# Performance work log

Measured on AMD Instinct MI355X. Metric: run time of the kernel, lower is better.

The kernel has to match this reference:

```python
import jax, jax.numpy as jnp
import numpy as np

B, S, D, H = 4, 2048, 1024, 16
HD = D // H  # head_dim = 64


def setup_inputs() -> dict:
    key = jax.random.key(0)
    ks = jax.random.split(key, 11)
    s = 1.0 / np.sqrt(D)
    return {
        "Q": jax.random.normal(ks[0], (B, S, D), dtype=jnp.float32),
        "K": jax.random.normal(ks[1], (B, S, D), dtype=jnp.float32),
        "V": jax.random.normal(ks[2], (B, S, D), dtype=jnp.float32),
        "Wq": jax.random.normal(ks[3], (D, D), dtype=jnp.float32) * s,
        "bq": jnp.zeros((D,), dtype=jnp.float32),
        "Wk": jax.random.normal(ks[4], (D, D), dtype=jnp.float32) * s,
        "bk": jnp.zeros((D,), dtype=jnp.float32),
        "Wv": jax.random.normal(ks[5], (D, D), dtype=jnp.float32) * s,
        "bv": jnp.zeros((D,), dtype=jnp.float32),
        "Wo": jax.random.normal(ks[6], (D, D), dtype=jnp.float32) * s,
        "bo": jnp.zeros((D,), dtype=jnp.float32),
    }


def _split_heads(x):
    # [B, S, D] -> [B, H, S, HD]
    b, s, _ = x.shape
    return x.reshape(b, s, H, HD).transpose(0, 2, 1, 3)


def reference(Q, K, V, Wq, bq, Wk, bk, Wv, bv, Wo, bo):
    q = _split_heads(Q @ Wq + bq)  # [B,H,S,HD]
    k = _split_heads(K @ Wk + bk)
    v = _split_heads(V @ Wv + bv)
    scale = 1.0 / jnp.sqrt(jnp.float32(HD))
    scores = jnp.einsum('bhqd,bhkd->bhqk', q, k) * scale  # [B,H,S,S]
    attn = jax.nn.softmax(scores, axis=-1)
    out = jnp.einsum('bhqk,bhkd->bhqd', attn, v)  # [B,H,S,HD]
    out = out.transpose(0, 2, 1, 3).reshape(Q.shape[0], -1, D)  # [B,S,D]
    return out @ Wo + bo
```

## Files before the change

kernel.cpp:

```cpp
#include <hip/hip_runtime.h>
#include <hip/hip_bf16.h>

typedef unsigned short u16;
typedef unsigned int u32;
typedef u16 u16x4 __attribute__((ext_vector_type(4)));
typedef u16 u16x8 __attribute__((ext_vector_type(8)));
typedef u32 u32x4 __attribute__((ext_vector_type(4)));
typedef float f32x4 __attribute__((ext_vector_type(4)));
typedef float f32x16 __attribute__((ext_vector_type(16)));
typedef __bf16 bf16x8 __attribute__((ext_vector_type(8)));

#define MFMA16(A, B, C) __builtin_amdgcn_mfma_f32_16x16x32_bf16( \
    __builtin_bit_cast(bf16x8, (A)), __builtin_bit_cast(bf16x8, (B)), (C), 0, 0, 0)
#define MFMA32(A, B, C) __builtin_amdgcn_mfma_f32_32x32x16_bf16( \
    __builtin_bit_cast(bf16x8, (A)), __builtin_bit_cast(bf16x8, (B)), (C), 0, 0, 0)

__device__ __forceinline__ u16 f2bf(float f) {
    u32 u = __float_as_uint(f);
    u += 0x7fffu + ((u >> 16) & 1u);
    return (u16)(u >> 16);
}

__device__ __forceinline__ u32 cvtpk(float lo, float hi) {
    u32 d;
    asm("v_cvt_pk_bf16_f32 %0, %1, %2" : "=v"(d) : "v"(lo), "v"(hi));
    return d;
}

__device__ __forceinline__ void gll16(const void* g, void* l) {
    __builtin_amdgcn_global_load_lds(
        (const __attribute__((address_space(1))) void*)g,
        (__attribute__((address_space(3))) void*)l, 16, 0, 0);
}

__global__ void f2bf3(const float* __restrict__ a0, const float* __restrict__ a1,
                      const float* __restrict__ a2, u16* __restrict__ o0,
                      u16* __restrict__ o1, u16* __restrict__ o2, int n4) {
    const float* in = (blockIdx.y == 0) ? a0 : (blockIdx.y == 1) ? a1 : a2;
    u16* out = (blockIdx.y == 0) ? o0 : (blockIdx.y == 1) ? o1 : o2;
    int i = blockIdx.x * blockDim.x + threadIdx.x;
    int stride = gridDim.x * blockDim.x;
    for (; i < n4; i += stride) {
        float4 v = ((const float4*)in)[i];
        u16x4 o;
        o[0] = f2bf(v.x); o[1] = f2bf(v.y); o[2] = f2bf(v.z); o[3] = f2bf(v.w);
        ((u16x4*)out)[i] = o;
    }
}

__global__ void cvt_wt(const float* __restrict__ W0, const float* __restrict__ W1,
                       const float* __restrict__ W2, const float* __restrict__ W3,
                       u16* __restrict__ T0, u16* __restrict__ T1,
                       u16* __restrict__ T2, u16* __restrict__ T3) {
    const int z = blockIdx.z;
    const float* W = (z == 0) ? W0 : (z == 1) ? W1 : (z == 2) ? W2 : W3;
    u16* T = (z == 0) ? T0 : (z == 1) ? T1 : (z == 2) ? T2 : T3;
    __shared__ float tile[64][65];
    const int n0 = blockIdx.x * 64, k0 = blockIdx.y * 64;
    const int tx = threadIdx.x & 63, ty = threadIdx.x >> 6;
#pragma unroll
    for (int i = 0; i < 16; ++i) {
        int r = i * 4 + ty;
        tile[r][tx] = W[(size_t)(k0 + r) * 1024 + n0 + tx];
    }
    __syncthreads();
#pragma unroll
    for (int i = 0; i < 16; ++i) {
        int r = i * 4 + ty;
        T[(size_t)(n0 + r) * 1024 + k0 + tx] = f2bf(tile[tx][r]);
    }
}

__device__ __forceinline__ void gemm_core(
    const u16* __restrict__ A, const u16* __restrict__ Bt,
    const float* __restrict__ bias, void* __restrict__ out,
    int mode, float scale, int bm, int bn, u16* lAs, u16* lBs) {
    const int tid = threadIdx.x, lane = tid & 63, wid = tid >> 6;
    const int wr = wid >> 1, wc = wid & 1;
    const int l15 = lane & 15, l16 = lane >> 4;

    f32x4 acc[4][4];
#pragma unroll
    for (int i = 0; i < 4; ++i)
#pragma unroll
        for (int j = 0; j < 4; ++j) acc[i][j] = f32x4{0.f, 0.f, 0.f, 0.f};

    const char* Ab = (const char*)A;
    const char* Bb = (const char*)Bt;
    char* ldsA = (char*)lAs;
    char* ldsB = (char*)lBs;
    const int rA0 = (wid * 4) * 8 + (lane >> 3);
    const int ci = ((lane & 7) ^ (lane >> 3)) * 16;

    for (int k0 = 0; k0 < 1024; k0 += 64) {
        __syncthreads();
#pragma unroll
        for (int c = 0; c < 4; ++c) {
            int row = rA0 + c * 8;
            gll16(Ab + ((size_t)(bm + row) * 1024 + k0) * 2 + ci, ldsA + (wid * 4 + c) * 1024);
            gll16(Bb + ((size_t)(bn + row) * 1024 + k0) * 2 + ci, ldsB + (wid * 4 + c) * 1024);
        }
        asm volatile("s_waitcnt vmcnt(0)" ::: "memory");
        __syncthreads();

#pragma unroll
        for (int kk = 0; kk < 2; ++kk) {
            u16x8 af[4], bf[4];
#pragma unroll
            for (int mi = 0; mi < 4; ++mi) {
                int row = wr * 64 + mi * 16 + l15;
                int cg = kk * 4 + l16;
                af[mi] = *(const u16x8*)(ldsA + row * 128 + ((cg ^ (row & 7)) * 16));
            }
#pragma unroll
            for (int ni = 0; ni < 4; ++ni) {
                int row = wc * 64 + ni * 16 + l15;
                int cg = kk * 4 + l16;
                bf[ni] = *(const u16x8*)(ldsB + row * 128 + ((cg ^ (row & 7)) * 16));
            }
#pragma unroll
            for (int mi = 0; mi < 4; ++mi)
#pragma unroll
                for (int ni = 0; ni < 4; ++ni)
                    acc[mi][ni] = MFMA16(af[mi], bf[ni], acc[mi][ni]);
        }
    }

    const int row0 = bm + wr * 64, col0 = bn + wc * 64;
#pragma unroll
    for (int ni = 0; ni < 4; ++ni) {
        int col = col0 + ni * 16 + l15;
        float bv = bias[col];
#pragma unroll
        for (int mi = 0; mi < 4; ++mi) {
#pragma unroll
            for (int r = 0; r < 4; ++r) {
                int row = row0 + mi * 16 + l16 * 4 + r;
                float v = (acc[mi][ni][r] + bv) * scale;
                if (mode == 2) {
                    ((float*)out)[(size_t)row * 1024 + col] = v;
                } else if (mode == 0) {
                    int b = row >> 11, s = row & 2047, h = col >> 6, d = col & 63;
                    ((u16*)out)[(((size_t)(b * 16 + h)) * 2048 + s) * 64 + d] = f2bf(v);
                } else {
                    int b = row >> 11, s = row & 2047, h = col >> 6, d = col & 63;
                    ((u16*)out)[(((size_t)(b * 16 + h)) * 64 + d) * 2048 + s] = f2bf(v);
                }
            }
        }
    }
}

__device__ __forceinline__ void xcd_decode(int wg, int& bm, int& bn) {
    int xcd = wg & 7, pos = wg >> 3;
    bm = (xcd * 8 + (pos >> 3)) * 128;
    bn = (pos & 7) * 128;
}

__global__ __launch_bounds__(256, 3) void gemm_qkv(
    const u16* __restrict__ XQ, const u16* __restrict__ XK, const u16* __restrict__ XV,
    const u16* __restrict__ WQ, const u16* __restrict__ WK, const u16* __restrict__ WV,
    const float* __restrict__ bq, const float* __restrict__ bk, const float* __restrict__ bv,
    u16* __restrict__ qo, u16* __restrict__ ko, u16* __restrict__ vo, float qscale) {
    __shared__ u16 lAs[128 * 64];
    __shared__ u16 lBs[128 * 64];
    const int z = blockIdx.z;
    const u16* A = (z == 0) ? XQ : (z == 1) ? XK : XV;
    const u16* Bt = (z == 0) ? WQ : (z == 1) ? WK : WV;
    const float* bias = (z == 0) ? bq : (z == 1) ? bk : bv;
    u16* out = (z == 0) ? qo : (z == 1) ? ko : vo;
    const int mode = (z == 2) ? 1 : 0;
    const float scale = (z == 0) ? qscale : 1.0f;
    int bm, bn;
    xcd_decode(blockIdx.y * 8 + blockIdx.x, bm, bn);
    gemm_core(A, Bt, bias, out, mode, scale, bm, bn, lAs, lBs);
}

__global__ __launch_bounds__(256, 3) void gemm_out(
    const u16* __restrict__ A, const u16* __restrict__ Bt,
    const float* __restrict__ bias, float* __restrict__ out) {
    __shared__ u16 lAs[128 * 64];
    __shared__ u16 lBs[128 * 64];
    int bm, bn;
    xcd_decode(blockIdx.y * 8 + blockIdx.x, bm, bn);
    gemm_core(A, Bt, bias, out, 2, 1.0f, bm, bn, lAs, lBs);
}

__global__ __launch_bounds__(256, 4) void attn_fwd(
    const u16* __restrict__ qh, const u16* __restrict__ kh,
    const u16* __restrict__ vth, u16* __restrict__ ao) {
    __shared__ u16 lK[2][64 * 64];
    __shared__ u16 lV[2][64 * 64];
    const int tid = threadIdx.x, lane = tid & 63, wid = tid >> 6;
    const int l31 = lane & 31, l32 = lane >> 5;
    const int wg = blockIdx.x;
    const int xcd = wg & 7, pos = wg >> 3;
    const int bh = xcd * 8 + (pos >> 4);
    const int xblk = pos & 15;
    const int q0 = xblk * 128 + wid * 32;
    const char* kb = (const char*)(kh + (size_t)bh * 2048 * 64);
    const char* vb = (const char*)(vth + (size_t)bh * 64 * 2048);
    const u16* qb = qh + (size_t)bh * 2048 * 64;

    u16x8 qf[4];
#pragma unroll
    for (int kc = 0; kc < 4; ++kc)
        qf[kc] = *(const u16x8*)(qb + (size_t)(q0 + l31) * 64 + kc * 16 + l32 * 8);

    float m_run = 0.f, l_run = 0.f;
    f32x16 oacc[2] = {};

    char* ldsK = (char*)lK;
    char* ldsV = (char*)lV;
    const int srow = wid * 16 + (lane >> 3);
    const int sci = ((lane & 7) ^ (lane >> 3)) * 16;

#define STAGE(kv0, bo) do { \
    _Pragma("unroll") \
    for (int c = 0; c < 2; ++c) { \
        int row = srow + c * 8; \
        gll16(kb + (size_t)((kv0) + row) * 128 + sci, ldsK + (bo) + (wid * 2 + c) * 1024); \
        gll16(vb + (size_t)row * 4096 + (size_t)(kv0) * 2 + sci, ldsV + (bo) + (wid * 2 + c) * 1024); \
    } } while (0)

    STAGE(0, 0);
    int cur = 0;

    for (int it = 0; it < 32; ++it) {
        if (it < 31) {
            STAGE((it + 1) * 64, (cur ^ 1) * 8192);
            asm volatile("s_waitcnt vmcnt(4)" ::: "memory");
        } else {
            asm volatile("s_waitcnt vmcnt(0)" ::: "memory");
        }
        __syncthreads();
        const char* K_ = ldsK + cur * 8192;
        const char* V_ = ldsV + cur * 8192;

        f32x16 s[2] = {};
        __builtin_amdgcn_s_setprio(1);
#pragma unroll
        for (int kc = 0; kc < 4; ++kc) {
#pragma unroll
            for (int sub = 0; sub < 2; ++sub) {
                int row = sub * 32 + l31;
                int cg = kc * 2 + l32;
                u16x8 kf = *(const u16x8*)(K_ + row * 128 + ((cg ^ (row & 7)) * 16));
                s[sub] = MFMA32(kf, qf[kc], s[sub]);
            }
        }
        __builtin_amdgcn_s_setprio(0);

        float p0[16], p1[16];
#pragma unroll
        for (int r = 0; r < 16; ++r) p0[r] = __builtin_amdgcn_exp2f(s[0][r] - m_run);
#pragma unroll
        for (int r = 0; r < 16; ++r) p1[r] = __builtin_amdgcn_exp2f(s[1][r] - m_run);

        float t8[8];
#pragma unroll
        for (int i = 0; i < 8; ++i)
            t8[i] = fmaxf(fmaxf(s[0][i], s[0][i + 8]), fmaxf(s[1][i], s[1][i + 8]));
        float pm = fmaxf(fmaxf(fmaxf(t8[0], t8[4]), fmaxf(t8[1], t8[5])),
                         fmaxf(fmaxf(t8[2], t8[6]), fmaxf(t8[3], t8[7])));
        pm = fmaxf(pm, __shfl_xor(pm, 32));

        if (!__all(pm <= m_run + 8.f)) {
            float mnew = fmaxf(m_run, pm);
            float f = __builtin_amdgcn_exp2f(m_run - mnew);
            m_run = mnew;
            l_run *= f;
#pragma unroll
            for (int r = 0; r < 16; ++r) p0[r] = __builtin_amdgcn_exp2f(s[0][r] - mnew);
#pragma unroll
            for (int r = 0; r < 16; ++r) p1[r] = __builtin_amdgcn_exp2f(s[1][r] - mnew);
#pragma unroll
            for (int r = 0; r < 16; ++r) {
                int rq = ((r & 3) + 8 * (r >> 2)) + 4 * l32;
                float fr = __shfl(f, rq);
                oacc[0][r] *= fr;
                oacc[1][r] *= fr;
            }
        }

        u16x8 pa[2][2];
#pragma unroll
        for (int c2 = 0; c2 < 2; ++c2) {
            u32 x0 = cvtpk(p0[c2 * 8 + 0], p0[c2 * 8 + 1]);
            u32 x1 = cvtpk(p0[c2 * 8 + 2], p0[c2 * 8 + 3]);
            u32 y0 = cvtpk(p0[c2 * 8 + 4], p0[c2 * 8 + 5]);
            u32 y1 = cvtpk(p0[c2 * 8 + 6], p0[c2 * 8 + 7]);
            asm("v_permlane32_swap_b32 %0, %1" : "+v"(x0), "+v"(y0));
            asm("v_permlane32_swap_b32 %0, %1" : "+v"(x1), "+v"(y1));
            u32x4 wa = {x0, x1, y0, y1};
            pa[0][c2] = __builtin_bit_cast(u16x8, wa);
            u32 z0 = cvtpk(p1[c2 * 8 + 0], p1[c2 * 8 + 1]);
            u32 z1 = cvtpk(p1[c2 * 8 + 2], p1[c2 * 8 + 3]);
            u32 v0 = cvtpk(p1[c2 * 8 + 4], p1[c2 * 8 + 5]);
            u32 v1 = cvtpk(p1[c2 * 8 + 6], p1[c2 * 8 + 7]);
            asm("v_permlane32_swap_b32 %0, %1" : "+v"(z0), "+v"(v0));
            asm("v_permlane32_swap_b32 %0, %1" : "+v"(z1), "+v"(v1));
            u32x4 wb = {z0, z1, v0, v1};
            pa[1][c2] = __builtin_bit_cast(u16x8, wb);
        }

        float a8[8];
#pragma unroll
        for (int i = 0; i < 8; ++i)
            a8[i] = (p0[i] + p0[i + 8]) + (p1[i] + p1[i + 8]);
        float ls = ((a8[0] + a8[4]) + (a8[1] + a8[5])) +
                   ((a8[2] + a8[6]) + (a8[3] + a8[7]));
        ls += __shfl_xor(ls, 32);
        l_run += ls;

        __builtin_amdgcn_s_setprio(1);
#pragma unroll
        for (int dsub = 0; dsub < 2; ++dsub) {
#pragma unroll
            for (int sub = 0; sub < 2; ++sub) {
#pragma unroll
                for (int c2 = 0; c2 < 2; ++c2) {
                    int row = dsub * 32 + l31;
                    int cg = sub * 4 + c2 * 2 + l32;
                    u16x8 vf = *(const u16x8*)(V_ + row * 128 + ((cg ^ (row & 7)) * 16));
                    oacc[dsub] = MFMA32(pa[sub][c2], vf, oacc[dsub]);
                }
            }
        }
        __builtin_amdgcn_s_setprio(0);
        __syncthreads();
        cur ^= 1;
    }
#undef STAGE

    const int b = bh >> 4, h = bh & 15;
    float inv = 1.f / l_run;
#pragma unroll
    for (int r = 0; r < 16; ++r) {
        int rq = ((r & 3) + 8 * (r >> 2)) + 4 * l32;
        float fr = __shfl(inv, rq);
        int sq = q0 + rq;
#pragma unroll
        for (int dsub = 0; dsub < 2; ++dsub) {
            int d = dsub * 32 + l31;
            ao[((size_t)(b * 2048 + sq)) * 1024 + h * 64 + d] = f2bf(oacc[dsub][r] * fr);
        }
    }
}

extern "C" void kernel_launch(void* const* d_in, const int* in_sizes, int n_in,
                              void* d_out, int out_size, void* d_ws, size_t ws_size,
                              hipStream_t stream) {
    const float* Q  = (const float*)d_in[0];
    const float* K  = (const float*)d_in[1];
    const float* V  = (const float*)d_in[2];
    const float* Wq = (const float*)d_in[3];
    const float* bq = (const float*)d_in[4];
    const float* Wk = (const float*)d_in[5];
    const float* bk = (const float*)d_in[6];
    const float* Wv = (const float*)d_in[7];
    const float* bv = (const float*)d_in[8];
    const float* Wo = (const float*)d_in[9];
    const float* bo = (const float*)d_in[10];

    char* ws = (char*)d_ws;
    const size_t MB = 1024u * 1024u;
    u16* XQ  = (u16*)(ws);
    u16* XK  = (u16*)(ws + 16 * MB);
    u16* XV  = (u16*)(ws + 32 * MB);
    u16* WTQ = (u16*)(ws + 48 * MB);
    u16* WTK = (u16*)(ws + 50 * MB);
    u16* WTV = (u16*)(ws + 52 * MB);
    u16* WTO = (u16*)(ws + 54 * MB);
    u16* qhp = (u16*)(ws + 56 * MB);
    u16* khp = (u16*)(ws + 72 * MB);
    u16* vtp = (u16*)(ws + 88 * MB);
    u16* aop = XQ;

    const float qscale = 0.125f * 1.44269504088896f;

    f2bf3<<<dim3(2048, 3), 256, 0, stream>>>(Q, K, V, XQ, XK, XV, 2097152);
    cvt_wt<<<dim3(16, 16, 4), 256, 0, stream>>>(Wq, Wk, Wv, Wo, WTQ, WTK, WTV, WTO);

    gemm_qkv<<<dim3(8, 64, 3), 256, 0, stream>>>(XQ, XK, XV, WTQ, WTK, WTV,
                                                 bq, bk, bv, qhp, khp, vtp, qscale);

    attn_fwd<<<1024, 256, 0, stream>>>(qhp, khp, vtp, aop);

    gemm_out<<<dim3(8, 64), 256, 0, stream>>>(aop, WTO, bo, (float*)d_out);
}
```

Measured before the change: 213.2 us.

## Rewrite projection GEMMs as 8-wave 256x128 tiles with double-buffered LDS pipeline

The QKV and output projection GEMMs move from 4-wave 128x128 blocks with a single-buffered load/sync loop to 8-wave 256x128 blocks. Global-to-LDS loads for the next K tile are double-buffered and interleaved with MFMA phases using barriers and s_setprio. The goal is to hide global load latency behind matrix math and to reuse each B tile across more rows. In exchange it uses 96KB of LDS per block, allows one block per CU, and relies on a fixed barrier schedule that leaves less occupancy to hide stalls.

```diff
diff --git a/kernel.cpp b/kernel.cpp
--- a/kernel.cpp
+++ b/kernel.cpp
@@ -71,60 +71,87 @@
     }
 }
 
-__device__ __forceinline__ void gemm_core(
+__device__ __forceinline__ void gemm8_core(
     const u16* __restrict__ A, const u16* __restrict__ Bt,
     const float* __restrict__ bias, void* __restrict__ out,
-    int mode, float scale, int bm, int bn, u16* lAs, u16* lBs) {
+    int mode, float scale, int bm, int bn, char* ldsA, char* ldsB) {
     const int tid = threadIdx.x, lane = tid & 63, wid = tid >> 6;
     const int wr = wid >> 1, wc = wid & 1;
     const int l15 = lane & 15, l16 = lane >> 4;
-
-    f32x4 acc[4][4];
-#pragma unroll
-    for (int i = 0; i < 4; ++i)
-#pragma unroll
-        for (int j = 0; j < 4; ++j) acc[i][j] = f32x4{0.f, 0.f, 0.f, 0.f};
-
     const char* Ab = (const char*)A;
     const char* Bb = (const char*)Bt;
-    char* ldsA = (char*)lAs;
-    char* ldsB = (char*)lBs;
-    const int rA0 = (wid * 4) * 8 + (lane >> 3);
-    const int ci = ((lane & 7) ^ (lane >> 3)) * 16;
-
-    for (int k0 = 0; k0 < 1024; k0 += 64) {
-        __syncthreads();
-#pragma unroll
-        for (int c = 0; c < 4; ++c) {
-            int row = rA0 + c * 8;
-            gll16(Ab + ((size_t)(bm + row) * 1024 + k0) * 2 + ci, ldsA + (wid * 4 + c) * 1024);
-            gll16(Bb + ((size_t)(bn + row) * 1024 + k0) * 2 + ci, ldsB + (wid * 4 + c) * 1024);
-        }
-        asm volatile("s_waitcnt vmcnt(0)" ::: "memory");
-        __syncthreads();
-
-#pragma unroll
-        for (int kk = 0; kk < 2; ++kk) {
-            u16x8 af[4], bf[4];
-#pragma unroll
-            for (int mi = 0; mi < 4; ++mi) {
-                int row = wr * 64 + mi * 16 + l15;
-                int cg = kk * 4 + l16;
-                af[mi] = *(const u16x8*)(ldsA + row * 128 + ((cg ^ (row & 7)) * 16));
-            }
-#pragma unroll
-            for (int ni = 0; ni < 4; ++ni) {
-                int row = wc * 64 + ni * 16 + l15;
-                int cg = kk * 4 + l16;
-                bf[ni] = *(const u16x8*)(ldsB + row * 128 + ((cg ^ (row & 7)) * 16));
-            }
-#pragma unroll
-            for (int mi = 0; mi < 4; ++mi)
-#pragma unroll
-                for (int ni = 0; ni < 4; ++ni)
-                    acc[mi][ni] = MFMA16(af[mi], bf[ni], acc[mi][ni]);
-        }
-    }
+    const int srow8 = wid * 8 + (lane >> 3);
+    const int sc = ((lane & 7) ^ (lane >> 3)) * 16;
+
+    f32x4 acc[4][4];
+#pragma unroll
+    for (int i = 0; i < 4; ++i)
+#pragma unroll
+        for (int j = 0; j < 4; ++j) acc[i][j] = f32x4{0.f, 0.f, 0.f, 0.f};
+
+#define SA_(t, d, c) gll16(Ab + ((size_t)(bm + (c) * 64 + srow8) * 1024 + (t) * 64) * 2 + sc, \
+                           ldsA + (d) * 32768 + (c) * 8192 + wid * 1024)
+#define SB_(t, d, c) gll16(Bb + ((size_t)(bn + (c) * 64 + srow8) * 1024 + (t) * 64) * 2 + sc, \
+                           ldsB + (d) * 16384 + (c) * 8192 + wid * 1024)
+#define LDA_(d, kk, dst) _Pragma("unroll") \
+    for (int mi = 0; mi < 4; ++mi) { \
+        int row = wr * 64 + mi * 16 + l15; \
+        int cg = (kk) * 4 + l16; \
+        dst[mi] = *(const u16x8*)(ldsA + (d) * 32768 + row * 128 + ((cg ^ (row & 7)) * 16)); }
+#define LDB_(d, kk, dst) _Pragma("unroll") \
+    for (int ni = 0; ni < 4; ++ni) { \
+        int row = wc * 64 + ni * 16 + l15; \
+        int cg = (kk) * 4 + l16; \
+        dst[ni] = *(const u16x8*)(ldsB + (d) * 16384 + row * 128 + ((cg ^ (row & 7)) * 16)); }
+#define MM_(af, bf, nh) _Pragma("unroll") \
+    for (int mi = 0; mi < 4; ++mi) \
+        _Pragma("unroll") for (int nj = 0; nj < 2; ++nj) \
+            acc[mi][(nh) * 2 + nj] = MFMA16(af[mi], bf[(nh) * 2 + nj], acc[mi][(nh) * 2 + nj]);
+
+#define HALF_(d, tp) do { \
+    asm volatile("s_waitcnt vmcnt(0)" ::: "memory"); \
+    __builtin_amdgcn_s_barrier(); \
+    __builtin_amdgcn_sched_barrier(0); \
+    u16x8 a0[4], b0[4], a1[4], b1[4]; \
+    LDA_(d, 0, a0); LDB_(d, 0, b0); \
+    if ((tp) < 16) { SA_(tp, (d) ^ 1, 0); SA_(tp, (d) ^ 1, 1); } \
+    __builtin_amdgcn_s_barrier(); \
+    __builtin_amdgcn_s_setprio(1); \
+    MM_(a0, b0, 0); \
+    __builtin_amdgcn_s_setprio(0); \
+    __builtin_amdgcn_s_barrier(); \
+    LDA_(d, 1, a1); LDB_(d, 1, b1); \
+    if ((tp) < 16) { SA_(tp, (d) ^ 1, 2); SA_(tp, (d) ^ 1, 3); } \
+    __builtin_amdgcn_s_barrier(); \
+    __builtin_amdgcn_s_setprio(1); \
+    MM_(a0, b0, 1); \
+    __builtin_amdgcn_s_setprio(0); \
+    __builtin_amdgcn_s_barrier(); \
+    if ((tp) < 16) { SB_(tp, (d) ^ 1, 0); SB_(tp, (d) ^ 1, 1); } \
+    __builtin_amdgcn_s_barrier(); \
+    __builtin_amdgcn_s_setprio(1); \
+    MM_(a1, b1, 0); \
+    __builtin_amdgcn_s_setprio(0); \
+    __builtin_amdgcn_s_barrier(); \
+    __builtin_amdgcn_s_setprio(1); \
+    MM_(a1, b1, 1); \
+    __builtin_amdgcn_s_setprio(0); \
+    __builtin_amdgcn_s_barrier(); \
+} while (0)
+
+    SA_(0, 0, 0); SA_(0, 0, 1); SA_(0, 0, 2); SA_(0, 0, 3);
+    SB_(0, 0, 0); SB_(0, 0, 1);
+
+    for (int i = 0; i < 8; ++i) {
+        HALF_(0, 2 * i + 1);
+        HALF_(1, 2 * i + 2);
+    }
+#undef HALF_
+#undef MM_
+#undef LDB_
+#undef LDA_
+#undef SB_
+#undef SA_
 
     const int row0 = bm + wr * 64, col0 = bn + wc * 64;
 #pragma unroll
@@ -151,20 +178,20 @@
     }
 }
 
-__device__ __forceinline__ void xcd_decode(int wg, int& bm, int& bn) {
+__device__ __forceinline__ void xcd_decode256(int wg, int& bm, int& bn) {
     int xcd = wg & 7, pos = wg >> 3;
-    bm = (xcd * 8 + (pos >> 3)) * 128;
+    bm = (xcd * 4 + (pos >> 3)) * 256;
     bn = (pos & 7) * 128;
 }
 
-__global__ __launch_bounds__(256, 3) void gemm_qkv(
+__global__ __launch_bounds__(512, 1) void gemm_qkv(
     const u16* __restrict__ XQ, const u16* __restrict__ XK, const u16* __restrict__ XV,
     const u16* __restrict__ WQ, const u16* __restrict__ WK, const u16* __restrict__ WV,
     const float* __restrict__ bq, const float* __restrict__ bk, const float* __restrict__ bv,
     u16* __restrict__ qo, u16* __restrict__ ko, u16* __restrict__ vo, float qscale) {
-    __shared__ u16 lAs[128 * 64];
-    __shared__ u16 lBs[128 * 64];
-    const int z = blockIdx.z;
+    __shared__ char ldsA[65536];
+    __shared__ char ldsB[32768];
+    const int z = blockIdx.y;
     const u16* A = (z == 0) ? XQ : (z == 1) ? XK : XV;
     const u16* Bt = (z == 0) ? WQ : (z == 1) ? WK : WV;
     const float* bias = (z == 0) ? bq : (z == 1) ? bk : bv;
@@ -172,18 +199,18 @@
     const int mode = (z == 2) ? 1 : 0;
     const float scale = (z == 0) ? qscale : 1.0f;
     int bm, bn;
-    xcd_decode(blockIdx.y * 8 + blockIdx.x, bm, bn);
-    gemm_core(A, Bt, bias, out, mode, scale, bm, bn, lAs, lBs);
-}
-
-__global__ __launch_bounds__(256, 3) void gemm_out(
+    xcd_decode256(blockIdx.x, bm, bn);
+    gemm8_core(A, Bt, bias, out, mode, scale, bm, bn, ldsA, ldsB);
+}
+
+__global__ __launch_bounds__(512, 1) void gemm_out(
     const u16* __restrict__ A, const u16* __restrict__ Bt,
     const float* __restrict__ bias, float* __restrict__ out) {
-    __shared__ u16 lAs[128 * 64];
-    __shared__ u16 lBs[128 * 64];
+    __shared__ char ldsA[65536];
+    __shared__ char ldsB[32768];
     int bm, bn;
-    xcd_decode(blockIdx.y * 8 + blockIdx.x, bm, bn);
-    gemm_core(A, Bt, bias, out, 2, 1.0f, bm, bn, lAs, lBs);
+    xcd_decode256(blockIdx.x, bm, bn);
+    gemm8_core(A, Bt, bias, out, 2, 1.0f, bm, bn, ldsA, ldsB);
 }
 
 __global__ __launch_bounds__(256, 4) void attn_fwd(
@@ -382,10 +409,10 @@
     f2bf3<<<dim3(2048, 3), 256, 0, stream>>>(Q, K, V, XQ, XK, XV, 2097152);
     cvt_wt<<<dim3(16, 16, 4), 256, 0, stream>>>(Wq, Wk, Wv, Wo, WTQ, WTK, WTV, WTO);
 
-    gemm_qkv<<<dim3(8, 64, 3), 256, 0, stream>>>(XQ, XK, XV, WTQ, WTK, WTV,
-                                                 bq, bk, bv, qhp, khp, vtp, qscale);
+    gemm_qkv<<<dim3(256, 3), 512, 0, stream>>>(XQ, XK, XV, WTQ, WTK, WTV,
+                                               bq, bk, bv, qhp, khp, vtp, qscale);
 
     attn_fwd<<<1024, 256, 0, stream>>>(qhp, khp, vtp, aop);
 
-    gemm_out<<<dim3(8, 64), 256, 0, stream>>>(aop, WTO, bo, (float*)d_out);
-}
+    gemm_out<<<256, 512, 0, stream>>>(aop, WTO, bo, (float*)d_out);
+}
```

Result: slower. 224.3 us (+5.2%).

## Fuse fp32-to-bf16 activation conversion into QKV GEMM tile loads

Applied to the files above, without the earlier changes.

Removes the separate f2bf3 pass that converted Q/K/V activations to bf16. The QKV GEMM now loads the fp32 activations directly with vector loads, packs them to bf16 with v_cvt_pk_bf16_f32, and stores them into LDS in the same swizzled layout. This saves one full write and read of the bf16 activation copies and one kernel launch. In exchange, each GEMM tile reads fp32 (twice the bytes) and the A loads are no longer asynchronous global_load_lds, and activations are reloaded by every N-column block.

```diff
diff --git a/kernel.cpp b/kernel.cpp
--- a/kernel.cpp
+++ b/kernel.cpp
@@ -31,21 +31,6 @@
     __builtin_amdgcn_global_load_lds(
         (const __attribute__((address_space(1))) void*)g,
         (__attribute__((address_space(3))) void*)l, 16, 0, 0);
-}
-
-__global__ void f2bf3(const float* __restrict__ a0, const float* __restrict__ a1,
-                      const float* __restrict__ a2, u16* __restrict__ o0,
-                      u16* __restrict__ o1, u16* __restrict__ o2, int n4) {
-    const float* in = (blockIdx.y == 0) ? a0 : (blockIdx.y == 1) ? a1 : a2;
-    u16* out = (blockIdx.y == 0) ? o0 : (blockIdx.y == 1) ? o1 : o2;
-    int i = blockIdx.x * blockDim.x + threadIdx.x;
-    int stride = gridDim.x * blockDim.x;
-    for (; i < n4; i += stride) {
-        float4 v = ((const float4*)in)[i];
-        u16x4 o;
-        o[0] = f2bf(v.x); o[1] = f2bf(v.y); o[2] = f2bf(v.z); o[3] = f2bf(v.w);
-        ((u16x4*)out)[i] = o;
-    }
 }
 
 __global__ void cvt_wt(const float* __restrict__ W0, const float* __restrict__ W1,
@@ -71,8 +56,9 @@
     }
 }
 
+template <bool F32A>
 __device__ __forceinline__ void gemm_core(
-    const u16* __restrict__ A, const u16* __restrict__ Bt,
+    const void* __restrict__ Aptr, const u16* __restrict__ Bt,
     const float* __restrict__ bias, void* __restrict__ out,
     int mode, float scale, int bm, int bn, u16* lAs, u16* lBs) {
     const int tid = threadIdx.x, lane = tid & 63, wid = tid >> 6;
@@ -85,19 +71,31 @@
 #pragma unroll
         for (int j = 0; j < 4; ++j) acc[i][j] = f32x4{0.f, 0.f, 0.f, 0.f};
 
-    const char* Ab = (const char*)A;
+    const char* Ab = (const char*)Aptr;
+    const float* A32 = (const float*)Aptr;
     const char* Bb = (const char*)Bt;
     char* ldsA = (char*)lAs;
     char* ldsB = (char*)lBs;
-    const int rA0 = (wid * 4) * 8 + (lane >> 3);
-    const int ci = ((lane & 7) ^ (lane >> 3)) * 16;
+    const int rA0 = wid * 32 + (lane >> 3);
+    const int se = ((lane & 7) ^ (lane >> 3)) * 8;
+    const int ci = se * 2;
 
     for (int k0 = 0; k0 < 1024; k0 += 64) {
         __syncthreads();
 #pragma unroll
         for (int c = 0; c < 4; ++c) {
             int row = rA0 + c * 8;
-            gll16(Ab + ((size_t)(bm + row) * 1024 + k0) * 2 + ci, ldsA + (wid * 4 + c) * 1024);
+            if (F32A) {
+                const float* src = A32 + (size_t)(bm + row) * 1024 + k0 + se;
+                float4 fa = *(const float4*)src;
+                float4 fb = *(const float4*)(src + 4);
+                u32x4 pk = {cvtpk(fa.x, fa.y), cvtpk(fa.z, fa.w),
+                            cvtpk(fb.x, fb.y), cvtpk(fb.z, fb.w)};
+                *(u32x4*)(ldsA + (wid * 4 + c) * 1024 + lane * 16) = pk;
+            } else {
+                gll16(Ab + ((size_t)(bm + row) * 1024 + k0) * 2 + ci,
+                      ldsA + (wid * 4 + c) * 1024);
+            }
             gll16(Bb + ((size_t)(bn + row) * 1024 + k0) * 2 + ci, ldsB + (wid * 4 + c) * 1024);
         }
         asm volatile("s_waitcnt vmcnt(0)" ::: "memory");
@@ -158,14 +156,14 @@
 }
 
 __global__ __launch_bounds__(256, 3) void gemm_qkv(
-    const u16* __restrict__ XQ, const u16* __restrict__ XK, const u16* __restrict__ XV,
+    const float* __restrict__ Qf, const float* __restrict__ Kf, const float* __restrict__ Vf,
     const u16* __restrict__ WQ, const u16* __restrict__ WK, const u16* __restrict__ WV,
     const float* __restrict__ bq, const float* __restrict__ bk, const float* __restrict__ bv,
     u16* __restrict__ qo, u16* __restrict__ ko, u16* __restrict__ vo, float qscale) {
     __shared__ u16 lAs[128 * 64];
     __shared__ u16 lBs[128 * 64];
     const int z = blockIdx.z;
-    const u16* A = (z == 0) ? XQ : (z == 1) ? XK : XV;
+    const float* A = (z == 0) ? Qf : (z == 1) ? Kf : Vf;
     const u16* Bt = (z == 0) ? WQ : (z == 1) ? WK : WV;
     const float* bias = (z == 0) ? bq : (z == 1) ? bk : bv;
     u16* out = (z == 0) ? qo : (z == 1) ? ko : vo;
@@ -173,7 +171,7 @@
     const float scale = (z == 0) ? qscale : 1.0f;
     int bm, bn;
     xcd_decode(blockIdx.y * 8 + blockIdx.x, bm, bn);
-    gemm_core(A, Bt, bias, out, mode, scale, bm, bn, lAs, lBs);
+    gemm_core<true>(A, Bt, bias, out, mode, scale, bm, bn, lAs, lBs);
 }
 
 __global__ __launch_bounds__(256, 3) void gemm_out(
@@ -183,7 +181,7 @@
     __shared__ u16 lBs[128 * 64];
     int bm, bn;
     xcd_decode(blockIdx.y * 8 + blockIdx.x, bm, bn);
-    gemm_core(A, Bt, bias, out, 2, 1.0f, bm, bn, lAs, lBs);
+    gemm_core<false>(A, Bt, bias, out, 2, 1.0f, bm, bn, lAs, lBs);
 }
 
 __global__ __launch_bounds__(256, 4) void attn_fwd(
@@ -365,24 +363,20 @@
 
     char* ws = (char*)d_ws;
     const size_t MB = 1024u * 1024u;
-    u16* XQ  = (u16*)(ws);
-    u16* XK  = (u16*)(ws + 16 * MB);
-    u16* XV  = (u16*)(ws + 32 * MB);
-    u16* WTQ = (u16*)(ws + 48 * MB);
-    u16* WTK = (u16*)(ws + 50 * MB);
-    u16* WTV = (u16*)(ws + 52 * MB);
-    u16* WTO = (u16*)(ws + 54 * MB);
-    u16* qhp = (u16*)(ws + 56 * MB);
-    u16* khp = (u16*)(ws + 72 * MB);
-    u16* vtp = (u16*)(ws + 88 * MB);
-    u16* aop = XQ;
+    u16* WTQ = (u16*)(ws);
+    u16* WTK = (u16*)(ws + 2 * MB);
+    u16* WTV = (u16*)(ws + 4 * MB);
+    u16* WTO = (u16*)(ws + 6 * MB);
+    u16* qhp = (u16*)(ws + 8 * MB);
+    u16* khp = (u16*)(ws + 24 * MB);
+    u16* vtp = (u16*)(ws + 40 * MB);
+    u16* aop = (u16*)(ws + 56 * MB);
 
     const float qscale = 0.125f * 1.44269504088896f;
 
-    f2bf3<<<dim3(2048, 3), 256, 0, stream>>>(Q, K, V, XQ, XK, XV, 2097152);
     cvt_wt<<<dim3(16, 16, 4), 256, 0, stream>>>(Wq, Wk, Wv, Wo, WTQ, WTK, WTV, WTO);
 
-    gemm_qkv<<<dim3(8, 64, 3), 256, 0, stream>>>(XQ, XK, XV, WTQ, WTK, WTV,
+    gemm_qkv<<<dim3(8, 64, 3), 256, 0, stream>>>(Q, K, V, WTQ, WTK, WTV,
                                                  bq, bk, bv, qhp, khp, vtp, qscale);
 
     attn_fwd<<<1024, 256, 0, stream>>>(qhp, khp, vtp, aop);
```

Result: slower. 220.7 us (+3.5%).
